# Kernel optimization log

Hardware: AMD Instinct MI355X
Metric: run time of the kernel (lower is better)

Reference implementation:

```python
import jax, jax.numpy as jnp
import numpy as np

V, BLK, D, H, L = 50257, 2048, 768, 12, 4
HD = D // H
EPS = 1e-5


def _ln(x, w, b):
    mu = jnp.mean(x, axis=-1, keepdims=True)
    var = jnp.mean(jnp.square(x - mu), axis=-1, keepdims=True)
    return (x - mu) * jax.lax.rsqrt(var + EPS) * w + b


def setup_inputs() -> dict:
    key = jax.random.key(0)
    ks = iter(jax.random.split(key, 32))
    s = 0.02
    idx = jax.random.randint(next(ks), (2, 2048), 0, V)
    inp = {
        "idx": idx,
        "wte": jax.random.normal(next(ks), (V, D), jnp.float32) * s,
        "wpe": jax.random.normal(next(ks), (BLK, D), jnp.float32) * s,
        # stacked per-layer params [L, ...]
        "ln1_w": jnp.ones((L, D), jnp.float32),
        "ln1_b": jnp.zeros((L, D), jnp.float32),
        "attn_w": jax.random.normal(next(ks), (L, D, 3 * D), jnp.float32) * s,
        "attn_b": jnp.zeros((L, 3 * D), jnp.float32),
        "proj_w": jax.random.normal(next(ks), (L, D, D), jnp.float32) * (s / np.sqrt(2 * L)),
        "proj_b": jnp.zeros((L, D), jnp.float32),
        "ln2_w": jnp.ones((L, D), jnp.float32),
        "ln2_b": jnp.zeros((L, D), jnp.float32),
        "fc_w": jax.random.normal(next(ks), (L, D, 4 * D), jnp.float32) * s,
        "fc_b": jnp.zeros((L, 4 * D), jnp.float32),
        "fcp_w": jax.random.normal(next(ks), (L, 4 * D, D), jnp.float32) * (s / np.sqrt(2 * L)),
        "fcp_b": jnp.zeros((L, D), jnp.float32),
        "lnf_w": jnp.ones((D,), jnp.float32),
        "lnf_b": jnp.zeros((D,), jnp.float32),
    }
    return inp


def _gpt_forward(idx, wte, wpe, ln1_w, ln1_b, attn_w, attn_b, proj_w, proj_b,
                 ln2_w, ln2_b, fc_w, fc_b, fcp_w, fcp_b, lnf_w, lnf_b):
    B, T = idx.shape
    x = wte[idx] + wpe[:T]  # [B,T,D]; dropout p=0 -> identity
    causal = jnp.tril(jnp.ones((T, T), bool))
    scale = 1.0 / np.sqrt(HD)

    def block(x, p):
        l1w, l1b, aw, ab, pw, pb, l2w, l2b, fw, fb, fpw, fpb = p
        h = _ln(x, l1w, l1b)
        qkv = h @ aw + ab  # [B,T,3D]
        q, k, v = jnp.split(qkv, 3, axis=-1)
        q = q.reshape(B, T, H, HD).transpose(0, 2, 1, 3)  # [B,H,T,hd]
        k = k.reshape(B, T, H, HD).transpose(0, 2, 1, 3)
        v = v.reshape(B, T, H, HD).transpose(0, 2, 1, 3)
        att = jnp.einsum('bhqd,bhkd->bhqk', q, k) * scale
        att = jnp.where(causal, att, -jnp.inf)
        att = jax.nn.softmax(att, axis=-1)
        y = jnp.einsum('bhqk,bhkd->bhqd', att, v)
        y = y.transpose(0, 2, 1, 3).reshape(B, T, D)
        x = x + y @ pw + pb
        h2 = _ln(x, l2w, l2b)
        m = jax.nn.gelu(h2 @ fw + fb, approximate=False) @ fpw + fpb
        return x + m, None

    params = (ln1_w, ln1_b, attn_w, attn_b, proj_w, proj_b,
              ln2_w, ln2_b, fc_w, fc_b, fcp_w, fcp_b)
    x, _ = jax.lax.scan(block, x, params)
    x = _ln(x, lnf_w, lnf_b)
    # inference path: logits only for last position, lm_head tied to wte
    logits = x[:, -1:, :] @ wte.T  # [B,1,V]
    return logits


def reference(idx, wte, wpe, ln1_w, ln1_b, attn_w, attn_b, proj_w, proj_b,
              ln2_w, ln2_b, fc_w, fc_b, fcp_w, fcp_b, lnf_w, lnf_b):
    return _gpt_forward(idx, wte, wpe, ln1_w, ln1_b, attn_w, attn_b, proj_w, proj_b,
                        ln2_w, ln2_b, fc_w, fc_b, fcp_w, fcp_b, lnf_w, lnf_b)
```

## Files before the change

### kernel.cpp

```cpp
#include <hip/hip_runtime.h>
#include <math.h>

#define V 50257
#define B 2
#define T 2048
#define D 768
#define H 12
#define HD 64
#define L 4
#define D3 (3*D)
#define D4 (4*D)
#define NTOK (B*T)
#define EPS 1e-5f

typedef __bf16 v8bf __attribute__((ext_vector_type(8)));
typedef __bf16 v4bf __attribute__((ext_vector_type(4)));
typedef unsigned short v8us __attribute__((ext_vector_type(8)));
typedef float  v4f  __attribute__((ext_vector_type(4)));

#define GAS(p) ((const __attribute__((address_space(1))) void*)(p))
#define LAS(p) ((__attribute__((address_space(3))) void*)(p))

#define LIDX(row, chunk) ((row)*64 + ((((chunk) ^ ((row)&7)))<<3))

__global__ __launch_bounds__(256) void prep_kernel(
        const int* __restrict__ idx, const float* __restrict__ wte,
        const float* __restrict__ wpe, float* __restrict__ x,
        const float* __restrict__ aw_all,  const float* __restrict__ pw_all,
        const float* __restrict__ fw_all,  const float* __restrict__ fpw_all,
        __bf16* __restrict__ awt_all, __bf16* __restrict__ pwt_all,
        __bf16* __restrict__ fwt_all, __bf16* __restrict__ fpwt_all) {
    int bid = blockIdx.x;
    if (bid < 3072) {
        int e = (bid * 256 + threadIdx.x) * 4;
        int pos = e / D;
        int d   = e - pos * D;
        int t   = pos & (T - 1);
        int tok = idx[pos];
        const float4 a  = *(const float4*)(wte + (size_t)tok * D + d);
        const float4 p4 = *(const float4*)(wpe + (size_t)t * D + d);
        float4 r; r.x = a.x + p4.x; r.y = a.y + p4.y; r.z = a.z + p4.z; r.w = a.w + p4.w;
        *(float4*)(x + e) = r;
        return;
    }
    bid -= 3072;
    const int l = bid / 6912; bid -= l * 6912;
    const float* W; __bf16* Wt; int K, N, bx, by;
    if (bid < 1728)      {             W = aw_all  + (size_t)l * D  * D3; Wt = awt_all  + (size_t)l * D3 * D;  K = D;  N = D3; bx = bid % 72; by = bid / 72; }
    else if (bid < 2304) { bid -= 1728; W = pw_all  + (size_t)l * D  * D;  Wt = pwt_all  + (size_t)l * D  * D;  K = D;  N = D;  bx = bid % 24; by = bid / 24; }
    else if (bid < 4608) { bid -= 2304; W = fw_all  + (size_t)l * D  * D4; Wt = fwt_all  + (size_t)l * D4 * D;  K = D;  N = D4; bx = bid % 96; by = bid / 96; }
    else                 { bid -= 4608; W = fpw_all + (size_t)l * D4 * D;  Wt = fpwt_all + (size_t)l * D  * D4; K = D4; N = D;  bx = bid % 24; by = bid / 24; }
    __shared__ float t[32][33];
    const int n0 = bx * 32, k0 = by * 32;
    const int tx = threadIdx.x & 31, ty = threadIdx.x >> 5;
    #pragma unroll
    for (int p = 0; p < 4; ++p)
        t[ty + 8 * p][tx] = W[(size_t)(k0 + ty + 8 * p) * N + n0 + tx];
    __syncthreads();
    #pragma unroll
    for (int p = 0; p < 4; ++p)
        Wt[(size_t)(n0 + ty + 8 * p) * K + k0 + tx] = (__bf16)t[tx][ty + 8 * p];
}

__global__ __launch_bounds__(256) void ln_kernel(const float* __restrict__ X,
                                                 const float* __restrict__ w,
                                                 const float* __restrict__ b,
                                                 __bf16* __restrict__ Y,
                                                 int src_mul, int src_off) {
    int srow = blockIdx.x * src_mul + src_off;
    const float* xr = X + (size_t)srow * D;
    float v[3];
    float s = 0.f, s2 = 0.f;
    #pragma unroll
    for (int j = 0; j < 3; ++j) {
        v[j] = xr[threadIdx.x + 256 * j];
        s += v[j];
        s2 += v[j] * v[j];
    }
    #pragma unroll
    for (int off = 32; off; off >>= 1) {
        s  += __shfl_xor(s, off);
        s2 += __shfl_xor(s2, off);
    }
    __shared__ float ss[4], ss2[4];
    int wave = threadIdx.x >> 6, lane = threadIdx.x & 63;
    if (lane == 0) { ss[wave] = s; ss2[wave] = s2; }
    __syncthreads();
    s  = ss[0] + ss[1] + ss[2] + ss[3];
    s2 = ss2[0] + ss2[1] + ss2[2] + ss2[3];
    float mu  = s * (1.f / D);
    float var = s2 * (1.f / D) - mu * mu;
    float rs  = rsqrtf(var + EPS);
    __bf16* yr = Y + (size_t)blockIdx.x * D;
    #pragma unroll
    for (int j = 0; j < 3; ++j) {
        int c = threadIdx.x + 256 * j;
        yr[c] = (__bf16)((v[j] - mu) * rs * w[c] + b[c]);
    }
}

template<bool OUTBF16, bool DOGELU, bool DORES>
__global__ __launch_bounds__(256) void gemm_bt(const __bf16* __restrict__ A,
                                               const __bf16* __restrict__ Wt,
                                               const float* __restrict__ bias,
                                               const float* __restrict__ res,
                                               void* __restrict__ Cout,
                                               int N, int K) {
    __shared__ __align__(16) __bf16 As[8192];
    __shared__ __align__(16) __bf16 Bs[8192];
    const int tid  = threadIdx.x;
    const int w    = tid >> 6;
    const int lane = tid & 63;
    const int row0 = blockIdx.y * 128;
    const int col0 = blockIdx.x * 128;

    const int c0   = tid;
    const int srow = ((c0 >> 6) & 3) * 16 + (c0 & 15);
    const int sk   = ((c0 >> 4) & 3) * 8;
    const __bf16* gA0 = A  + (size_t)(row0 + srow) * K + sk;
    const __bf16* gA1 = gA0 + (size_t)64 * K;
    const __bf16* gB0 = Wt + (size_t)(col0 + srow) * K + sk;
    const __bf16* gB1 = gB0 + (size_t)64 * K;
    __bf16* lA0 = As + (size_t)c0 * 8;
    __bf16* lA1 = As + (size_t)(c0 + 256) * 8;
    __bf16* lA2 = As + 4096 + (size_t)c0 * 8;
    __bf16* lA3 = As + 4096 + (size_t)(c0 + 256) * 8;
    __bf16* lB0 = Bs + (size_t)c0 * 8;
    __bf16* lB1 = Bs + (size_t)(c0 + 256) * 8;
    __bf16* lB2 = Bs + 4096 + (size_t)c0 * 8;
    __bf16* lB3 = Bs + 4096 + (size_t)(c0 + 256) * 8;

    const int wr = w >> 1, wc = w & 1;
    const __bf16* rA = As + wr * 2048 + lane * 8;
    const __bf16* rB = Bs + wc * 2048 + lane * 8;

    v4f acc[4][4] = {};
    for (int k0 = 0; k0 < K; k0 += 64) {
        __builtin_amdgcn_global_load_lds(GAS(gA0),      LAS(lA0), 16, 0, 0);
        __builtin_amdgcn_global_load_lds(GAS(gA1),      LAS(lA1), 16, 0, 0);
        __builtin_amdgcn_global_load_lds(GAS(gA0 + 32), LAS(lA2), 16, 0, 0);
        __builtin_amdgcn_global_load_lds(GAS(gA1 + 32), LAS(lA3), 16, 0, 0);
        __builtin_amdgcn_global_load_lds(GAS(gB0),      LAS(lB0), 16, 0, 0);
        __builtin_amdgcn_global_load_lds(GAS(gB1),      LAS(lB1), 16, 0, 0);
        __builtin_amdgcn_global_load_lds(GAS(gB0 + 32), LAS(lB2), 16, 0, 0);
        __builtin_amdgcn_global_load_lds(GAS(gB1 + 32), LAS(lB3), 16, 0, 0);
        gA0 += 64; gA1 += 64; gB0 += 64; gB1 += 64;
        __syncthreads();
        #pragma unroll
        for (int h = 0; h < 2; ++h) {
            v8bf af[4], bfr[4];
            #pragma unroll
            for (int i = 0; i < 4; ++i) af[i]  = *(const v8bf*)(rA + h * 4096 + i * 512);
            #pragma unroll
            for (int j = 0; j < 4; ++j) bfr[j] = *(const v8bf*)(rB + h * 4096 + j * 512);
            #pragma unroll
            for (int i = 0; i < 4; ++i)
                #pragma unroll
                for (int j = 0; j < 4; ++j)
                    acc[i][j] = __builtin_amdgcn_mfma_f32_16x16x32_bf16(af[i], bfr[j], acc[i][j], 0, 0, 0);
        }
        __syncthreads();
    }

    const int er = (lane >> 4) * 4;
    const int ec = lane & 15;
    #pragma unroll
    for (int j = 0; j < 4; ++j) {
        const int col = col0 + wc * 64 + j * 16 + ec;
        const float bval = bias[col];
        #pragma unroll
        for (int i = 0; i < 4; ++i) {
            #pragma unroll
            for (int rr = 0; rr < 4; ++rr) {
                const int row = row0 + wr * 64 + i * 16 + er + rr;
                float vv = acc[i][j][rr] + bval;
                if (DOGELU) vv = 0.5f * vv * (1.f + erff(vv * 0.70710678118f));
                if (DORES)  vv += res[(size_t)row * N + col];
                if (OUTBF16) ((__bf16*)Cout)[(size_t)row * N + col] = (__bf16)vv;
                else         ((float*) Cout)[(size_t)row * N + col] = vv;
            }
        }
    }
}

template<bool OUTBF16, bool DOGELU, bool DORES>
__global__ __launch_bounds__(256) void gemm_bt64(const __bf16* __restrict__ A,
                                                 const __bf16* __restrict__ Wt,
                                                 const float* __restrict__ bias,
                                                 const float* __restrict__ res,
                                                 void* __restrict__ Cout,
                                                 int N, int K) {
    __shared__ __align__(16) __bf16 As[8192];
    __shared__ __align__(16) __bf16 Bs[4096];
    const int tid  = threadIdx.x;
    const int w    = tid >> 6;
    const int lane = tid & 63;
    const int row0 = blockIdx.y * 128;
    const int col0 = blockIdx.x * 64;

    const int c0   = tid;
    const int srow = ((c0 >> 6) & 3) * 16 + (c0 & 15);
    const int sk   = ((c0 >> 4) & 3) * 8;
    const __bf16* gA0 = A  + (size_t)(row0 + srow) * K + sk;
    const __bf16* gA1 = gA0 + (size_t)64 * K;
    const __bf16* gB0 = Wt + (size_t)(col0 + srow) * K + sk;
    __bf16* lA0 = As + (size_t)c0 * 8;
    __bf16* lA1 = As + (size_t)(c0 + 256) * 8;
    __bf16* lA2 = As + 4096 + (size_t)c0 * 8;
    __bf16* lA3 = As + 4096 + (size_t)(c0 + 256) * 8;
    __bf16* lB0 = Bs + (size_t)c0 * 8;
    __bf16* lB1 = Bs + 2048 + (size_t)c0 * 8;

    const int wr = w >> 1, wc = w & 1;
    const __bf16* rA = As + wr * 2048 + lane * 8;
    const __bf16* rB = Bs + wc * 1024 + lane * 8;

    v4f acc[4][2] = {};
    for (int k0 = 0; k0 < K; k0 += 64) {
        __builtin_amdgcn_global_load_lds(GAS(gA0),      LAS(lA0), 16, 0, 0);
        __builtin_amdgcn_global_load_lds(GAS(gA1),      LAS(lA1), 16, 0, 0);
        __builtin_amdgcn_global_load_lds(GAS(gA0 + 32), LAS(lA2), 16, 0, 0);
        __builtin_amdgcn_global_load_lds(GAS(gA1 + 32), LAS(lA3), 16, 0, 0);
        __builtin_amdgcn_global_load_lds(GAS(gB0),      LAS(lB0), 16, 0, 0);
        __builtin_amdgcn_global_load_lds(GAS(gB0 + 32), LAS(lB1), 16, 0, 0);
        gA0 += 64; gA1 += 64; gB0 += 64;
        __syncthreads();
        #pragma unroll
        for (int h = 0; h < 2; ++h) {
            v8bf af[4], bfr[2];
            #pragma unroll
            for (int i = 0; i < 4; ++i) af[i]  = *(const v8bf*)(rA + h * 4096 + i * 512);
            #pragma unroll
            for (int j = 0; j < 2; ++j) bfr[j] = *(const v8bf*)(rB + h * 2048 + j * 512);
            #pragma unroll
            for (int i = 0; i < 4; ++i)
                #pragma unroll
                for (int j = 0; j < 2; ++j)
                    acc[i][j] = __builtin_amdgcn_mfma_f32_16x16x32_bf16(af[i], bfr[j], acc[i][j], 0, 0, 0);
        }
        __syncthreads();
    }

    const int er = (lane >> 4) * 4;
    const int ec = lane & 15;
    #pragma unroll
    for (int j = 0; j < 2; ++j) {
        const int col = col0 + wc * 32 + j * 16 + ec;
        const float bval = bias[col];
        #pragma unroll
        for (int i = 0; i < 4; ++i) {
            #pragma unroll
            for (int rr = 0; rr < 4; ++rr) {
                const int row = row0 + wr * 64 + i * 16 + er + rr;
                float vv = acc[i][j][rr] + bval;
                if (DOGELU) vv = 0.5f * vv * (1.f + erff(vv * 0.70710678118f));
                if (DORES)  vv += res[(size_t)row * N + col];
                if (OUTBF16) ((__bf16*)Cout)[(size_t)row * N + col] = (__bf16)vv;
                else         ((float*) Cout)[(size_t)row * N + col] = vv;
            }
        }
    }
}

__global__ __launch_bounds__(256) void attn_mfma(const __bf16* __restrict__ qkv,
                                                 __bf16* __restrict__ y) {
    __shared__ __align__(16) __bf16 Qs[4096];
    __shared__ __align__(16) __bf16 Ks[4096];
    __shared__ __align__(16) __bf16 Vt[4096];
    __shared__ __align__(16) __bf16 Ps[4][1024];

    const int tid  = threadIdx.x;
    const int w    = tid >> 6;
    const int lane = tid & 63;
    const int quad = lane >> 4;
    const int l4   = lane & 15;

    const int qt = 31 - (blockIdx.x & 31);
    const int bh = blockIdx.x >> 5;
    const int b  = bh / H;
    const int h  = bh - b * H;
    const int q0 = qt * 64;

    const __bf16* base = qkv + (size_t)(b * T) * D3 + h * HD;

    {
        int c = tid;
        #pragma unroll
        for (int rep = 0; rep < 2; ++rep, c += 256) {
            int row = c >> 3, ch = c & 7;
            v8us v = *(const v8us*)(const void*)(base + (size_t)(q0 + row) * D3 + ch * 8);
            *(v8us*)(void*)(Qs + LIDX(row, ch)) = v;
        }
    }

    const int krow = tid >> 3, kch = tid & 7;
    const int vkp = tid & 31, vdc = tid >> 5;
    const __bf16* kp0 = base + D     + (size_t)krow * D3 + kch * 8;
    const __bf16* kp1 = kp0 + (size_t)32 * D3;
    const __bf16* vp0 = base + 2 * D + (size_t)(2 * vkp) * D3 + vdc * 8;
    const __bf16* vp1 = vp0 + D3;

    v8us kr0 = *(const v8us*)(const void*)kp0;
    v8us kr1 = *(const v8us*)(const void*)kp1;
    v8us vr0 = *(const v8us*)(const void*)vp0;
    v8us vr1 = *(const v8us*)(const void*)vp1;

    float m_local = -INFINITY;
    v4f o[4] = {};
    v4f sacc = {};
    v8bf qf[2];
    v8bf vones;
    #pragma unroll
    for (int i = 0; i < 8; ++i) vones[i] = (__bf16)1.0f;

    const int nt = qt + 1;
    const size_t adv = (size_t)64 * D3;
    const int qrow = q0 + w * 16 + l4;

    for (int kt = 0; kt < nt; ++kt) {
        const int k0 = kt * 64;
        *(v8us*)(void*)(Ks + LIDX(krow, kch))      = kr0;
        *(v8us*)(void*)(Ks + LIDX(krow + 32, kch)) = kr1;
        #pragma unroll
        for (int j = 0; j < 8; ++j) {
            int dim = vdc * 8 + j;
            int idx = dim * 64 + ((((vkp >> 2) ^ (dim & 7))) << 3) + ((vkp & 3) << 1);
            *(unsigned int*)(void*)(Vt + idx) =
                ((unsigned int)vr1[j] << 16) | (unsigned int)vr0[j];
        }
        __syncthreads();

        if (kt == 0) {
            #pragma unroll
            for (int kh = 0; kh < 2; ++kh)
                qf[kh] = *(const v8bf*)(Qs + LIDX(w * 16 + l4, kh * 4 + quad));
        }
        if (kt + 1 < nt) {
            kp0 += adv; kp1 += adv; vp0 += adv; vp1 += adv;
            kr0 = *(const v8us*)(const void*)kp0;
            kr1 = *(const v8us*)(const void*)kp1;
            vr0 = *(const v8us*)(const void*)vp0;
            vr1 = *(const v8us*)(const void*)vp1;
        }

        v4f s[4] = {};
        __builtin_amdgcn_s_setprio(1);
        #pragma unroll
        for (int kh = 0; kh < 2; ++kh) {
            #pragma unroll
            for (int jb = 0; jb < 4; ++jb) {
                v8bf bk = *(const v8bf*)(Ks + LIDX(jb * 16 + l4, kh * 4 + quad));
                s[jb] = __builtin_amdgcn_mfma_f32_16x16x32_bf16(bk, qf[kh], s[jb], 0, 0, 0);
            }
        }
        __builtin_amdgcn_s_setprio(0);

        float sv[4][4];
        float mx = -INFINITY;
        #pragma unroll
        for (int jb = 0; jb < 4; ++jb) {
            #pragma unroll
            for (int rg = 0; rg < 4; ++rg) {
                float vvv = s[jb][rg] * 0.125f;
                if (k0 + jb * 16 + quad * 4 + rg > qrow) vvv = -INFINITY;
                sv[jb][rg] = vvv;
                mx = fmaxf(mx, vvv);
            }
        }
        mx = fmaxf(mx, __shfl_xor(mx, 16));
        mx = fmaxf(mx, __shfl_xor(mx, 32));
        if (!__all(mx <= m_local + 8.f)) {
            const float mnew    = fmaxf(m_local, mx);
            const float alpha_l = __expf(m_local - mnew);
            m_local = mnew;
            float a4[4];
            #pragma unroll
            for (int r = 0; r < 4; ++r) a4[r] = __shfl(alpha_l, quad * 4 + r);
            #pragma unroll
            for (int r = 0; r < 4; ++r) {
                sacc[r] *= a4[r];
                #pragma unroll
                for (int db = 0; db < 4; ++db) o[db][r] *= a4[r];
            }
        }
        #pragma unroll
        for (int jb = 0; jb < 4; ++jb) {
            v4bf pk;
            #pragma unroll
            for (int rg = 0; rg < 4; ++rg)
                pk[rg] = (__bf16)__expf(sv[jb][rg] - m_local);
            *(v4bf*)(void*)(&Ps[w][LIDX(l4, jb * 2 + (quad >> 1)) + ((quad & 1) << 2)]) = pk;
        }
        __builtin_amdgcn_s_setprio(1);
        #pragma unroll
        for (int kh = 0; kh < 2; ++kh) {
            v8bf ap = *(const v8bf*)(&Ps[w][LIDX(l4, kh * 4 + quad)]);
            sacc = __builtin_amdgcn_mfma_f32_16x16x32_bf16(ap, vones, sacc, 0, 0, 0);
            #pragma unroll
            for (int db = 0; db < 4; ++db) {
                v8bf bv = *(const v8bf*)(Vt + LIDX(db * 16 + l4, kh * 4 + quad));
                o[db] = __builtin_amdgcn_mfma_f32_16x16x32_bf16(ap, bv, o[db], 0, 0, 0);
            }
        }
        __builtin_amdgcn_s_setprio(0);
        __syncthreads();
    }

    #pragma unroll
    for (int db = 0; db < 4; ++db) {
        #pragma unroll
        for (int r = 0; r < 4; ++r) {
            const int q = q0 + w * 16 + quad * 4 + r;
            y[(size_t)(b * T + q) * D + h * HD + db * 16 + l4] =
                (__bf16)(o[db][r] / sacc[r]);
        }
    }
}

__global__ __launch_bounds__(256) void logits_kernel(const __bf16* __restrict__ xf,
                                                     const float* __restrict__ wte,
                                                     float* __restrict__ out) {
    int wave = threadIdx.x >> 6;
    int lane = threadIdx.x & 63;
    int v = blockIdx.x * 4 + wave;
    if (v >= V) return;
    const float4* wr = (const float4*)(wte + (size_t)v * D);
    const v4bf*   x0 = (const v4bf*)(xf);
    const v4bf*   x1 = (const v4bf*)(xf + D);
    float s0 = 0.f, s1 = 0.f;
    #pragma unroll
    for (int j = 0; j < 3; ++j) {
        float4 wv = wr[lane + 64 * j];
        v4bf a0 = x0[lane + 64 * j];
        v4bf a1 = x1[lane + 64 * j];
        s0 = fmaf(wv.x, (float)a0[0], s0); s0 = fmaf(wv.y, (float)a0[1], s0);
        s0 = fmaf(wv.z, (float)a0[2], s0); s0 = fmaf(wv.w, (float)a0[3], s0);
        s1 = fmaf(wv.x, (float)a1[0], s1); s1 = fmaf(wv.y, (float)a1[1], s1);
        s1 = fmaf(wv.z, (float)a1[2], s1); s1 = fmaf(wv.w, (float)a1[3], s1);
    }
    #pragma unroll
    for (int off = 32; off; off >>= 1) {
        s0 += __shfl_xor(s0, off);
        s1 += __shfl_xor(s1, off);
    }
    if (lane == 0) { out[v] = s0; out[V + v] = s1; }
}

extern "C" void kernel_launch(void* const* d_in, const int* in_sizes, int n_in,
                              void* d_out, int out_size, void* d_ws, size_t ws_size,
                              hipStream_t stream) {
    const int*   idx    = (const int*)  d_in[0];
    const float* wte    = (const float*)d_in[1];
    const float* wpe    = (const float*)d_in[2];
    const float* ln1_w  = (const float*)d_in[3];
    const float* ln1_b  = (const float*)d_in[4];
    const float* attn_w = (const float*)d_in[5];
    const float* attn_b = (const float*)d_in[6];
    const float* proj_w = (const float*)d_in[7];
    const float* proj_b = (const float*)d_in[8];
    const float* ln2_w  = (const float*)d_in[9];
    const float* ln2_b  = (const float*)d_in[10];
    const float* fc_w   = (const float*)d_in[11];
    const float* fc_b   = (const float*)d_in[12];
    const float* fcp_w  = (const float*)d_in[13];
    const float* fcp_b  = (const float*)d_in[14];
    const float* lnf_w  = (const float*)d_in[15];
    const float* lnf_b  = (const float*)d_in[16];
    float* out = (float*)d_out;

    char* ws = (char*)d_ws;
    float*  x    = (float*)ws;  ws += (size_t)NTOK * D  * 4;
    __bf16* qkvb = (__bf16*)ws;
    __bf16* gb   = (__bf16*)ws; ws += (size_t)NTOK * D4 * 2;
    __bf16* hb   = (__bf16*)ws; ws += (size_t)NTOK * D  * 2;
    __bf16* yb   = (__bf16*)ws; ws += (size_t)NTOK * D  * 2;
    __bf16* awt  = (__bf16*)ws; ws += (size_t)L * D3 * D   * 2;
    __bf16* pwt  = (__bf16*)ws; ws += (size_t)L * D  * D   * 2;
    __bf16* fwt  = (__bf16*)ws; ws += (size_t)L * D4 * D   * 2;
    __bf16* fpwt = (__bf16*)ws; ws += (size_t)L * D  * D4  * 2;
    __bf16* xf   = (__bf16*)ws; ws += (size_t)B * D    * 2;

    prep_kernel<<<3072 + 6912 * L, 256, 0, stream>>>(idx, wte, wpe, x,
                                                     attn_w, proj_w, fc_w, fcp_w,
                                                     awt, pwt, fwt, fpwt);

    for (int l = 0; l < L; ++l) {
        const float* l1w = ln1_w + l * D;
        const float* l1b = ln1_b + l * D;
        const float* ab  = attn_b + l * D3;
        const float* pb  = proj_b + l * D;
        const float* l2w = ln2_w + l * D;
        const float* l2b = ln2_b + l * D;
        const float* fb  = fc_b + l * D4;
        const float* fpb = fcp_b + l * D;
        const __bf16* awl  = awt  + (size_t)l * D3 * D;
        const __bf16* pwl  = pwt  + (size_t)l * D  * D;
        const __bf16* fwl  = fwt  + (size_t)l * D4 * D;
        const __bf16* fpwl = fpwt + (size_t)l * D  * D4;

        ln_kernel<<<NTOK, 256, 0, stream>>>(x, l1w, l1b, hb, 1, 0);
        gemm_bt<true, false, false><<<dim3(D3 / 128, NTOK / 128), 256, 0, stream>>>(
            hb, awl, ab, nullptr, qkvb, D3, D);
        attn_mfma<<<B * H * (T / 64), 256, 0, stream>>>(qkvb, yb);
        gemm_bt64<false, false, true><<<dim3(D / 64, NTOK / 128), 256, 0, stream>>>(
            yb, pwl, pb, x, x, D, D);
        ln_kernel<<<NTOK, 256, 0, stream>>>(x, l2w, l2b, hb, 1, 0);
        gemm_bt<true, true, false><<<dim3(D4 / 128, NTOK / 128), 256, 0, stream>>>(
            hb, fwl, fb, nullptr, gb, D4, D);
        gemm_bt64<false, false, true><<<dim3(D / 64, NTOK / 128), 256, 0, stream>>>(
            gb, fpwl, fpb, x, x, D, D4);
    }

    ln_kernel<<<B, 256, 0, stream>>>(x, lnf_w, lnf_b, xf, T, T - 1);
    logits_kernel<<<(V + 3) / 4, 256, 0, stream>>>(xf, wte, out);
}
```

Measured before the change: 1.334 ms.

## Double-buffer GEMM LDS loads, stage bf16 epilogue via LDS, shrink residual GEMM tiles

Both GEMM kernels now double-buffer their shared-memory tiles, so the global-to-LDS load of the next K slice is issued before the MFMA work on the current one, and each step needs one barrier instead of two. The bf16-output GEMM writes its results into a swizzled LDS tile and then stores them to global memory as 16-byte vectors instead of scattered scalar stores. The residual projection GEMMs switch to 64x64 tiles, which doubles the number of blocks to improve occupancy. The cost is smaller per-step K chunks in the 128x128 kernel, so fewer MFMAs sit between barriers.

```diff
diff --git a/kernel.cpp b/kernel.cpp
--- a/kernel.cpp
+++ b/kernel.cpp
@@ -22,6 +22,7 @@
 #define LAS(p) ((__attribute__((address_space(3))) void*)(p))
 
 #define LIDX(row, chunk) ((row)*64 + ((((chunk) ^ ((row)&7)))<<3))
+#define CIDX(row, chunk) ((row)*128 + ((((chunk) ^ ((row)&7)))<<3))
 
 __global__ __launch_bounds__(256) void prep_kernel(
         const int* __restrict__ idx, const float* __restrict__ wte,
@@ -99,66 +100,65 @@
     }
 }
 
-template<bool OUTBF16, bool DOGELU, bool DORES>
+template<bool DOGELU>
 __global__ __launch_bounds__(256) void gemm_bt(const __bf16* __restrict__ A,
                                                const __bf16* __restrict__ Wt,
                                                const float* __restrict__ bias,
-                                               const float* __restrict__ res,
-                                               void* __restrict__ Cout,
+                                               __bf16* __restrict__ Cout,
                                                int N, int K) {
-    __shared__ __align__(16) __bf16 As[8192];
-    __shared__ __align__(16) __bf16 Bs[8192];
+    __shared__ __align__(16) __bf16 sm[16384];
+    __bf16* As = sm;
+    __bf16* Bs = sm + 8192;
     const int tid  = threadIdx.x;
     const int w    = tid >> 6;
     const int lane = tid & 63;
     const int row0 = blockIdx.y * 128;
     const int col0 = blockIdx.x * 128;
 
-    const int c0   = tid;
-    const int srow = ((c0 >> 6) & 3) * 16 + (c0 & 15);
-    const int sk   = ((c0 >> 4) & 3) * 8;
+    const int srow = ((tid >> 6) & 3) * 16 + (tid & 15);
+    const int sk   = ((tid >> 4) & 3) * 8;
     const __bf16* gA0 = A  + (size_t)(row0 + srow) * K + sk;
     const __bf16* gA1 = gA0 + (size_t)64 * K;
     const __bf16* gB0 = Wt + (size_t)(col0 + srow) * K + sk;
     const __bf16* gB1 = gB0 + (size_t)64 * K;
-    __bf16* lA0 = As + (size_t)c0 * 8;
-    __bf16* lA1 = As + (size_t)(c0 + 256) * 8;
-    __bf16* lA2 = As + 4096 + (size_t)c0 * 8;
-    __bf16* lA3 = As + 4096 + (size_t)(c0 + 256) * 8;
-    __bf16* lB0 = Bs + (size_t)c0 * 8;
-    __bf16* lB1 = Bs + (size_t)(c0 + 256) * 8;
-    __bf16* lB2 = Bs + 4096 + (size_t)c0 * 8;
-    __bf16* lB3 = Bs + 4096 + (size_t)(c0 + 256) * 8;
+    __bf16* lA0 = As + (size_t)tid * 8;
+    __bf16* lA1 = As + (size_t)(tid + 256) * 8;
+    __bf16* lB0 = Bs + (size_t)tid * 8;
+    __bf16* lB1 = Bs + (size_t)(tid + 256) * 8;
 
     const int wr = w >> 1, wc = w & 1;
     const __bf16* rA = As + wr * 2048 + lane * 8;
     const __bf16* rB = Bs + wc * 2048 + lane * 8;
 
+    __builtin_amdgcn_global_load_lds(GAS(gA0), LAS(lA0), 16, 0, 0);
+    __builtin_amdgcn_global_load_lds(GAS(gA1), LAS(lA1), 16, 0, 0);
+    __builtin_amdgcn_global_load_lds(GAS(gB0), LAS(lB0), 16, 0, 0);
+    __builtin_amdgcn_global_load_lds(GAS(gB1), LAS(lB1), 16, 0, 0);
+    gA0 += 32; gA1 += 32; gB0 += 32; gB1 += 32;
+    __syncthreads();
+
     v4f acc[4][4] = {};
-    for (int k0 = 0; k0 < K; k0 += 64) {
-        __builtin_amdgcn_global_load_lds(GAS(gA0),      LAS(lA0), 16, 0, 0);
-        __builtin_amdgcn_global_load_lds(GAS(gA1),      LAS(lA1), 16, 0, 0);
-        __builtin_amdgcn_global_load_lds(GAS(gA0 + 32), LAS(lA2), 16, 0, 0);
-        __builtin_amdgcn_global_load_lds(GAS(gA1 + 32), LAS(lA3), 16, 0, 0);
-        __builtin_amdgcn_global_load_lds(GAS(gB0),      LAS(lB0), 16, 0, 0);
-        __builtin_amdgcn_global_load_lds(GAS(gB1),      LAS(lB1), 16, 0, 0);
-        __builtin_amdgcn_global_load_lds(GAS(gB0 + 32), LAS(lB2), 16, 0, 0);
-        __builtin_amdgcn_global_load_lds(GAS(gB1 + 32), LAS(lB3), 16, 0, 0);
-        gA0 += 64; gA1 += 64; gB0 += 64; gB1 += 64;
-        __syncthreads();
-        #pragma unroll
-        for (int h = 0; h < 2; ++h) {
-            v8bf af[4], bfr[4];
-            #pragma unroll
-            for (int i = 0; i < 4; ++i) af[i]  = *(const v8bf*)(rA + h * 4096 + i * 512);
-            #pragma unroll
-            for (int j = 0; j < 4; ++j) bfr[j] = *(const v8bf*)(rB + h * 4096 + j * 512);
-            #pragma unroll
-            for (int i = 0; i < 4; ++i)
-                #pragma unroll
-                for (int j = 0; j < 4; ++j)
-                    acc[i][j] = __builtin_amdgcn_mfma_f32_16x16x32_bf16(af[i], bfr[j], acc[i][j], 0, 0, 0);
-        }
+    const int nt = K >> 5;
+    for (int t = 0; t < nt; ++t) {
+        const int cb = (t & 1) * 4096;
+        if (t + 1 < nt) {
+            const int nb = ((t + 1) & 1) * 4096;
+            __builtin_amdgcn_global_load_lds(GAS(gA0), LAS(lA0 + nb), 16, 0, 0);
+            __builtin_amdgcn_global_load_lds(GAS(gA1), LAS(lA1 + nb), 16, 0, 0);
+            __builtin_amdgcn_global_load_lds(GAS(gB0), LAS(lB0 + nb), 16, 0, 0);
+            __builtin_amdgcn_global_load_lds(GAS(gB1), LAS(lB1 + nb), 16, 0, 0);
+            gA0 += 32; gA1 += 32; gB0 += 32; gB1 += 32;
+        }
+        v8bf af[4], bfr[4];
+        #pragma unroll
+        for (int i = 0; i < 4; ++i) af[i]  = *(const v8bf*)(rA + cb + i * 512);
+        #pragma unroll
+        for (int j = 0; j < 4; ++j) bfr[j] = *(const v8bf*)(rB + cb + j * 512);
+        #pragma unroll
+        for (int i = 0; i < 4; ++i)
+            #pragma unroll
+            for (int j = 0; j < 4; ++j)
+                acc[i][j] = __builtin_amdgcn_mfma_f32_16x16x32_bf16(af[i], bfr[j], acc[i][j], 0, 0, 0);
         __syncthreads();
     }
 
@@ -166,74 +166,89 @@
     const int ec = lane & 15;
     #pragma unroll
     for (int j = 0; j < 4; ++j) {
-        const int col = col0 + wc * 64 + j * 16 + ec;
-        const float bval = bias[col];
+        const int col = wc * 64 + j * 16 + ec;
+        const float bval = bias[col0 + col];
+        const int chunk = col >> 3, ce = col & 7;
         #pragma unroll
         for (int i = 0; i < 4; ++i) {
+            const int rowb = wr * 64 + i * 16 + er;
             #pragma unroll
             for (int rr = 0; rr < 4; ++rr) {
-                const int row = row0 + wr * 64 + i * 16 + er + rr;
                 float vv = acc[i][j][rr] + bval;
                 if (DOGELU) vv = 0.5f * vv * (1.f + erff(vv * 0.70710678118f));
-                if (DORES)  vv += res[(size_t)row * N + col];
-                if (OUTBF16) ((__bf16*)Cout)[(size_t)row * N + col] = (__bf16)vv;
-                else         ((float*) Cout)[(size_t)row * N + col] = vv;
+                sm[CIDX(rowb + rr, chunk) + ce] = (__bf16)vv;
             }
         }
     }
-}
-
-template<bool OUTBF16, bool DOGELU, bool DORES>
-__global__ __launch_bounds__(256) void gemm_bt64(const __bf16* __restrict__ A,
-                                                 const __bf16* __restrict__ Wt,
-                                                 const float* __restrict__ bias,
-                                                 const float* __restrict__ res,
-                                                 void* __restrict__ Cout,
-                                                 int N, int K) {
-    __shared__ __align__(16) __bf16 As[8192];
-    __shared__ __align__(16) __bf16 Bs[4096];
+    __syncthreads();
+    #pragma unroll
+    for (int c = 0; c < 8; ++c) {
+        const int chunkid = tid + c * 256;
+        const int row = chunkid >> 4;
+        const int cc  = chunkid & 15;
+        *(v8us*)(void*)(Cout + (size_t)(row0 + row) * N + col0 + cc * 8) =
+            *(const v8us*)(const void*)(sm + CIDX(row, cc));
+    }
+}
+
+__global__ __launch_bounds__(256) void gemm64(const __bf16* __restrict__ A,
+                                              const __bf16* __restrict__ Wt,
+                                              const float* __restrict__ bias,
+                                              const float* __restrict__ res,
+                                              float* __restrict__ Cout,
+                                              int N, int K) {
+    __shared__ __align__(16) __bf16 sm[16384];
+    __bf16* As = sm;
+    __bf16* Bs = sm + 8192;
     const int tid  = threadIdx.x;
     const int w    = tid >> 6;
     const int lane = tid & 63;
-    const int row0 = blockIdx.y * 128;
+    const int row0 = blockIdx.y * 64;
     const int col0 = blockIdx.x * 64;
 
-    const int c0   = tid;
-    const int srow = ((c0 >> 6) & 3) * 16 + (c0 & 15);
-    const int sk   = ((c0 >> 4) & 3) * 8;
+    const int srow = ((tid >> 7) & 3) * 16 + (tid & 15);
+    const int sk   = ((tid >> 4) & 7) * 8;
     const __bf16* gA0 = A  + (size_t)(row0 + srow) * K + sk;
-    const __bf16* gA1 = gA0 + (size_t)64 * K;
+    const __bf16* gA1 = gA0 + (size_t)32 * K;
     const __bf16* gB0 = Wt + (size_t)(col0 + srow) * K + sk;
-    __bf16* lA0 = As + (size_t)c0 * 8;
-    __bf16* lA1 = As + (size_t)(c0 + 256) * 8;
-    __bf16* lA2 = As + 4096 + (size_t)c0 * 8;
-    __bf16* lA3 = As + 4096 + (size_t)(c0 + 256) * 8;
-    __bf16* lB0 = Bs + (size_t)c0 * 8;
-    __bf16* lB1 = Bs + 2048 + (size_t)c0 * 8;
+    const __bf16* gB1 = gB0 + (size_t)32 * K;
+    __bf16* lA0 = As + (size_t)tid * 8;
+    __bf16* lA1 = As + (size_t)(tid + 256) * 8;
+    __bf16* lB0 = Bs + (size_t)tid * 8;
+    __bf16* lB1 = Bs + (size_t)(tid + 256) * 8;
 
     const int wr = w >> 1, wc = w & 1;
     const __bf16* rA = As + wr * 2048 + lane * 8;
-    const __bf16* rB = Bs + wc * 1024 + lane * 8;
-
-    v4f acc[4][2] = {};
-    for (int k0 = 0; k0 < K; k0 += 64) {
-        __builtin_amdgcn_global_load_lds(GAS(gA0),      LAS(lA0), 16, 0, 0);
-        __builtin_amdgcn_global_load_lds(GAS(gA1),      LAS(lA1), 16, 0, 0);
-        __builtin_amdgcn_global_load_lds(GAS(gA0 + 32), LAS(lA2), 16, 0, 0);
-        __builtin_amdgcn_global_load_lds(GAS(gA1 + 32), LAS(lA3), 16, 0, 0);
-        __builtin_amdgcn_global_load_lds(GAS(gB0),      LAS(lB0), 16, 0, 0);
-        __builtin_amdgcn_global_load_lds(GAS(gB0 + 32), LAS(lB1), 16, 0, 0);
-        gA0 += 64; gA1 += 64; gB0 += 64;
-        __syncthreads();
+    const __bf16* rB = Bs + wc * 2048 + lane * 8;
+
+    __builtin_amdgcn_global_load_lds(GAS(gA0), LAS(lA0), 16, 0, 0);
+    __builtin_amdgcn_global_load_lds(GAS(gA1), LAS(lA1), 16, 0, 0);
+    __builtin_amdgcn_global_load_lds(GAS(gB0), LAS(lB0), 16, 0, 0);
+    __builtin_amdgcn_global_load_lds(GAS(gB1), LAS(lB1), 16, 0, 0);
+    gA0 += 64; gA1 += 64; gB0 += 64; gB1 += 64;
+    __syncthreads();
+
+    v4f acc[2][2] = {};
+    const int nt = K >> 6;
+    for (int t = 0; t < nt; ++t) {
+        const int cb = (t & 1) * 4096;
+        if (t + 1 < nt) {
+            const int nb = ((t + 1) & 1) * 4096;
+            __builtin_amdgcn_global_load_lds(GAS(gA0), LAS(lA0 + nb), 16, 0, 0);
+            __builtin_amdgcn_global_load_lds(GAS(gA1), LAS(lA1 + nb), 16, 0, 0);
+            __builtin_amdgcn_global_load_lds(GAS(gB0), LAS(lB0 + nb), 16, 0, 0);
+            __builtin_amdgcn_global_load_lds(GAS(gB1), LAS(lB1 + nb), 16, 0, 0);
+            gA0 += 64; gA1 += 64; gB0 += 64; gB1 += 64;
+        }
         #pragma unroll
         for (int h = 0; h < 2; ++h) {
-            v8bf af[4], bfr[2];
-            #pragma unroll
-            for (int i = 0; i < 4; ++i) af[i]  = *(const v8bf*)(rA + h * 4096 + i * 512);
-            #pragma unroll
-            for (int j = 0; j < 2; ++j) bfr[j] = *(const v8bf*)(rB + h * 2048 + j * 512);
-            #pragma unroll
-            for (int i = 0; i < 4; ++i)
+            v8bf af[2], bfr[2];
+            #pragma unroll
+            for (int i = 0; i < 2; ++i) af[i]  = *(const v8bf*)(rA + cb + i * 1024 + h * 512);
+            #pragma unroll
+            for (int j = 0; j < 2; ++j) bfr[j] = *(const v8bf*)(rB + cb + j * 1024 + h * 512);
+            #pragma unroll
+            for (int i = 0; i < 2; ++i)
                 #pragma unroll
                 for (int j = 0; j < 2; ++j)
                     acc[i][j] = __builtin_amdgcn_mfma_f32_16x16x32_bf16(af[i], bfr[j], acc[i][j], 0, 0, 0);
@@ -248,15 +263,11 @@
         const int col = col0 + wc * 32 + j * 16 + ec;
         const float bval = bias[col];
         #pragma unroll
-        for (int i = 0; i < 4; ++i) {
+        for (int i = 0; i < 2; ++i) {
             #pragma unroll
             for (int rr = 0; rr < 4; ++rr) {
-                const int row = row0 + wr * 64 + i * 16 + er + rr;
-                float vv = acc[i][j][rr] + bval;
-                if (DOGELU) vv = 0.5f * vv * (1.f + erff(vv * 0.70710678118f));
-                if (DORES)  vv += res[(size_t)row * N + col];
-                if (OUTBF16) ((__bf16*)Cout)[(size_t)row * N + col] = (__bf16)vv;
-                else         ((float*) Cout)[(size_t)row * N + col] = vv;
+                const int row = row0 + wr * 32 + i * 16 + er + rr;
+                Cout[(size_t)row * N + col] = acc[i][j][rr] + bval + res[(size_t)row * N + col];
             }
         }
     }
@@ -499,15 +510,15 @@
         const __bf16* fpwl = fpwt + (size_t)l * D  * D4;
 
         ln_kernel<<<NTOK, 256, 0, stream>>>(x, l1w, l1b, hb, 1, 0);
-        gemm_bt<true, false, false><<<dim3(D3 / 128, NTOK / 128), 256, 0, stream>>>(
-            hb, awl, ab, nullptr, qkvb, D3, D);
+        gemm_bt<false><<<dim3(D3 / 128, NTOK / 128), 256, 0, stream>>>(
+            hb, awl, ab, qkvb, D3, D);
         attn_mfma<<<B * H * (T / 64), 256, 0, stream>>>(qkvb, yb);
-        gemm_bt64<false, false, true><<<dim3(D / 64, NTOK / 128), 256, 0, stream>>>(
+        gemm64<<<dim3(D / 64, NTOK / 64), 256, 0, stream>>>(
             yb, pwl, pb, x, x, D, D);
         ln_kernel<<<NTOK, 256, 0, stream>>>(x, l2w, l2b, hb, 1, 0);
-        gemm_bt<true, true, false><<<dim3(D4 / 128, NTOK / 128), 256, 0, stream>>>(
-            hb, fwl, fb, nullptr, gb, D4, D);
-        gemm_bt64<false, false, true><<<dim3(D / 64, NTOK / 128), 256, 0, stream>>>(
+        gemm_bt<true><<<dim3(D4 / 128, NTOK / 128), 256, 0, stream>>>(
+            hb, fwl, fb, gb, D4, D);
+        gemm64<<<dim3(D / 64, NTOK / 64), 256, 0, stream>>>(
             gb, fpwl, fpb, x, x, D, D4);
     }
 
```

Result: faster. 1.286 ms (-3.6%).
